# Optimization experiments

Hardware: AMD Instinct MI355X
Metric: run time of the kernel (lower is better)

Reference implementation:

```python
import jax, jax.numpy as jnp
import numpy as np

B, N, M, D = 8, 512, 64, 128
H = 64  # mlp_hidden_dim


def setup_inputs() -> dict:
    key = jax.random.key(0)
    ks = jax.random.split(key, 10)
    op_emb = jax.random.normal(ks[0], (B, N, D), dtype=jnp.float32)
    machine_emb = jax.random.normal(ks[1], (B, M, D), dtype=jnp.float32)
    edge_emb = jax.random.normal(ks[2], (B, N, M, D), dtype=jnp.float32)
    action_mask = jax.random.randint(ks[3], (B, N, M), 0, 2) > 0
    s1 = 1.0 / np.sqrt(3 * D)
    s2 = 1.0 / np.sqrt(H)
    W1 = jax.random.uniform(ks[4], (3 * D, H), jnp.float32, -s1, s1)
    b1 = jax.random.uniform(ks[5], (H,), jnp.float32, -s1, s1)
    W2 = jax.random.uniform(ks[6], (H, H), jnp.float32, -s2, s2)
    b2 = jax.random.uniform(ks[7], (H,), jnp.float32, -s2, s2)
    W3 = jax.random.uniform(ks[8], (H, 1), jnp.float32, -s2, s2)
    b3 = jax.random.uniform(ks[9], (1,), jnp.float32, -s2, s2)
    return {"op_emb": op_emb, "machine_emb": machine_emb, "edge_emb": edge_emb,
            "action_mask": action_mask,
            "W1": W1, "b1": b1, "W2": W2, "b2": b2, "W3": W3, "b3": b3}


def reference(op_emb, machine_emb, edge_emb, action_mask, W1, b1, W2, b2, W3, b3):
    # Split first linear over the three concat chunks to avoid materializing
    # the (B,N,M,3D) concat tensor (same math as cat -> Linear).
    Wo, Wm, We = W1[:D], W1[D:2 * D], W1[2 * D:]
    h = (jnp.einsum('bnd,dh->bnh', op_emb, Wo)[:, :, None, :]
         + jnp.einsum('bmd,dh->bmh', machine_emb, Wm)[:, None, :, :]
         + jnp.einsum('bnmd,dh->bnmh', edge_emb, We) + b1)  # (B,N,M,H)
    h = jax.nn.relu(h)
    h = jax.nn.relu(h @ W2 + b2)
    scores = (h @ W3 + b3)[..., 0]  # (B,N,M)
    scores = jnp.where(action_mask, scores, -jnp.inf)
    return jax.nn.log_softmax(scores.reshape(B, N * M), axis=-1)
```

## Files before the change

kernel.cpp:

```cpp
#include <hip/hip_runtime.h>
#include <math.h>

#define Bb 8
#define Nn 512
#define Mm 64
#define Dd 128
#define Hh 64
#define Gg 8
#define NEG_BIG (-1.0e30f)

typedef __bf16 bf16x8 __attribute__((ext_vector_type(8)));
typedef float  f32x4  __attribute__((ext_vector_type(4)));

#define WS_WEB   0u
#define WS_W2B   16384u
#define WS_CWSF  24576u
#define WS_AOP   155648u
#define WS_SCORE 1204224u
#define WS_PART  2252800u

#define GLOAD_LDS(gp, lp) __builtin_amdgcn_global_load_lds( \
    (const __attribute__((address_space(1))) void*)(gp),    \
    (__attribute__((address_space(3))) void*)(lp), 16, 0, 0)

__global__ __launch_bounds__(256) void prep_kernel(
    const float* __restrict__ W1, const float* __restrict__ W2,
    const float* __restrict__ op_emb, const float* __restrict__ machine_emb,
    const float* __restrict__ b1, char* __restrict__ ws)
{
    if (blockIdx.x < 48) {
        __bf16* WeB = (__bf16*)(ws + WS_WEB);
        __bf16* W2B = (__bf16*)(ws + WS_W2B);
        int idx = blockIdx.x * 256 + threadIdx.x;
        if (idx < 8192) {
            int fid = idx >> 9, rem = idx & 511;
            int lane = rem >> 3, j = rem & 7;
            int t = fid >> 2, ks = fid & 3;
            int q = lane >> 4, ln = lane & 15;
            int d = ks * 32 + q * 8 + j;
            int h = t * 16 + ln;
            WeB[idx] = (__bf16)W1[(size_t)(2 * Dd + d) * Hh + h];
        } else {
            int i2 = idx - 8192;
            int fid = i2 >> 9, rem = i2 & 511;
            int lane = rem >> 3, j = rem & 7;
            int t = fid >> 1, ks = fid & 1;
            int q = lane >> 4, ln = lane & 15;
            int k = ks * 32 + q * 8 + j;
            int h = t * 16 + ln;
            W2B[i2] = (__bf16)W2[(size_t)k * Hh + h];
        }
        return;
    }
    float* CwsF = (float*)(ws + WS_CWSF);
    float* Aop  = (float*)(ws + WS_AOP);
    const int bid = (blockIdx.x - 48) * 4 + (threadIdx.x >> 6);
    const int h = threadIdx.x & 63;
    if (bid < Bb * Mm) {
        const float* mg = machine_emb + (size_t)bid * Dd;
        const float* Wm = W1 + (size_t)Dd * Hh;
        float acc = b1[h];
#pragma unroll 8
        for (int d = 0; d < Dd; ++d) acc = fmaf(mg[d], Wm[d * Hh + h], acc);
        int b = bid >> 6, m = bid & 63;
        int wq = m >> 4, q = (m >> 2) & 3, r = m & 3;
        int t = h >> 4, ln = h & 15;
        CwsF[((((b * 4 + wq) * 4 + t) * 64) + (q * 16 + ln)) * 4 + r] = acc;
    } else {
        const int bn = bid - Bb * Mm;
        const float* og = op_emb + (size_t)bn * Dd;
        float acc = 0.f;
#pragma unroll 8
        for (int d = 0; d < Dd; ++d) acc = fmaf(og[d], W1[d * Hh + h], acc);
        Aop[(size_t)bn * Hh + h] = acc;
    }
}

__global__ __launch_bounds__(256, 2) void main_kernel(
    const float* __restrict__ edge_emb, const int* __restrict__ mask,
    const float* __restrict__ b2, const float* __restrict__ W3,
    const float* __restrict__ b3, char* __restrict__ ws)
{
    __shared__ float  sEdge[4 * 2 * 2048];
    __shared__ float  sAop[Gg * Hh];
    __shared__ int    sMask[Gg * Mm];
    __shared__ __bf16 sH1[Mm * 72];
    __shared__ float  sRed[8];

    float* scores = (float*)(ws + WS_SCORE);
    float* part   = (float*)(ws + WS_PART);

    const int tid  = threadIdx.x;
    const int lane = tid & 63;
    const int w    = tid >> 6;
    const int q    = lane >> 4;
    const int ln   = lane & 15;
    const int bn0  = blockIdx.x * Gg;
    const int b    = bn0 >> 9;
    const int wu   = __builtin_amdgcn_readfirstlane(w);

    const float* ebase = edge_emb + ((size_t)bn0 * Mm + w * 16 + ln) * Dd + q * 8;

    {
        float* d0 = &sEdge[(wu * 2 + 0) * 2048];
        float* d1 = &sEdge[(wu * 2 + 1) * 2048];
#pragma unroll
        for (int s = 0; s < 8; ++s)
            GLOAD_LDS(ebase + (s >> 1) * 32 + (s & 1) * 4, d0 + s * 256);
#pragma unroll
        for (int s = 0; s < 8; ++s)
            GLOAD_LDS(ebase + 8192 + (s >> 1) * 32 + (s & 1) * 4, d1 + s * 256);
    }

    if (tid < 128) {
        ((f32x4*)sAop)[tid] = ((const f32x4*)(ws + WS_AOP))[(size_t)bn0 * 16 + tid];
        ((int4*)sMask)[tid] = ((const int4*)mask)[(size_t)bn0 * 16 + tid];
    }

    bf16x8 weF[16], w2F[8];
    f32x4  cv[4];
    {
        const bf16x8* WeB = (const bf16x8*)(ws + WS_WEB);
        const bf16x8* W2B = (const bf16x8*)(ws + WS_W2B);
#pragma unroll
        for (int f = 0; f < 16; ++f) weF[f] = WeB[f * 64 + lane];
#pragma unroll
        for (int f = 0; f < 8; ++f)  w2F[f] = W2B[f * 64 + lane];
        const f32x4* CwsF = (const f32x4*)(ws + WS_CWSF) + (size_t)b * 1024;
#pragma unroll
        for (int t = 0; t < 4; ++t)  cv[t] = CwsF[(w * 4 + t) * 64 + lane];
    }

    float b2v[4], w3v[4];
#pragma unroll
    for (int t = 0; t < 4; ++t) { b2v[t] = b2[t * 16 + ln]; w3v[t] = W3[t * 16 + ln]; }
    const float bias3 = b3[0];

    float m_loc = NEG_BIG, l_loc = 0.f;

    __syncthreads();

#pragma unroll
    for (int g = 0; g < Gg; ++g) {
        const int buf = g & 1;
        const float* ldsrd = &sEdge[(wu * 2 + buf) * 2048];

        if (g == Gg - 1) __builtin_amdgcn_s_waitcnt(0x0F70);
        else             __builtin_amdgcn_s_waitcnt(0x0F78);

        f32x4 lo[4], hi[4];
#pragma unroll
        for (int ks = 0; ks < 4; ++ks) {
            lo[ks] = *(const f32x4*)&ldsrd[(ks * 2 + 0) * 256 + lane * 4];
            hi[ks] = *(const f32x4*)&ldsrd[(ks * 2 + 1) * 256 + lane * 4];
        }
        bf16x8 af[4];
#pragma unroll
        for (int ks = 0; ks < 4; ++ks) {
            bf16x8 a;
            a[0] = (__bf16)lo[ks][0]; a[1] = (__bf16)lo[ks][1];
            a[2] = (__bf16)lo[ks][2]; a[3] = (__bf16)lo[ks][3];
            a[4] = (__bf16)hi[ks][0]; a[5] = (__bf16)hi[ks][1];
            a[6] = (__bf16)hi[ks][2]; a[7] = (__bf16)hi[ks][3];
            af[ks] = a;
        }

        if (g + 2 < Gg) {
            float* dst = &sEdge[(wu * 2 + buf) * 2048];
            const float* src = ebase + (size_t)(g + 2) * 8192;
#pragma unroll
            for (int s = 0; s < 8; ++s)
                GLOAD_LDS(src + (s >> 1) * 32 + (s & 1) * 4, dst + s * 256);
        }

        f32x4 acc[4];
#pragma unroll
        for (int t = 0; t < 4; ++t) {
            float av = sAop[g * Hh + t * 16 + ln];
            acc[t][0] = cv[t][0] + av; acc[t][1] = cv[t][1] + av;
            acc[t][2] = cv[t][2] + av; acc[t][3] = cv[t][3] + av;
        }

#pragma unroll
        for (int t = 0; t < 4; ++t)
#pragma unroll
            for (int ks = 0; ks < 4; ++ks)
                acc[t] = __builtin_amdgcn_mfma_f32_16x16x32_bf16(af[ks], weF[t * 4 + ks], acc[t], 0, 0, 0);

#pragma unroll
        for (int t = 0; t < 4; ++t)
#pragma unroll
            for (int r = 0; r < 4; ++r)
                sH1[(w * 16 + q * 4 + r) * 72 + t * 16 + ln] =
                    (__bf16)fmaxf(acc[t][r], 0.f);

        bf16x8 a2[2];
#pragma unroll
        for (int ks = 0; ks < 2; ++ks)
            a2[ks] = *(const bf16x8*)&sH1[(w * 16 + ln) * 72 + ks * 32 + q * 8];
        f32x4 c2[4];
#pragma unroll
        for (int t = 0; t < 4; ++t) c2[t] = (f32x4){0.f, 0.f, 0.f, 0.f};
#pragma unroll
        for (int t = 0; t < 4; ++t)
#pragma unroll
            for (int ks = 0; ks < 2; ++ks)
                c2[t] = __builtin_amdgcn_mfma_f32_16x16x32_bf16(a2[ks], w2F[t * 2 + ks], c2[t], 0, 0, 0);

        float p[4] = {0.f, 0.f, 0.f, 0.f};
#pragma unroll
        for (int t = 0; t < 4; ++t)
#pragma unroll
            for (int r = 0; r < 4; ++r)
                p[r] += fmaxf(c2[t][r] + b2v[t], 0.f) * w3v[t];
#pragma unroll
        for (int r = 0; r < 4; ++r) {
            p[r] += __shfl_xor(p[r], 1, 64);
            p[r] += __shfl_xor(p[r], 2, 64);
            p[r] += __shfl_xor(p[r], 4, 64);
            p[r] += __shfl_xor(p[r], 8, 64);
        }
        const int m0 = w * 16 + q * 4;
        const int* mrow = &sMask[g * Mm + m0];
        float vv[4];
#pragma unroll
        for (int r = 0; r < 4; ++r) {
            float v = p[r] + bias3;
            vv[r] = mrow[r] ? v : NEG_BIG;
            if (mrow[r]) {
                float mn = fmaxf(m_loc, v);
                l_loc = l_loc * expf(m_loc - mn) + expf(v - mn);
                m_loc = mn;
            }
        }
        if (ln == 0) {
            float4 o; o.x = vv[0]; o.y = vv[1]; o.z = vv[2]; o.w = vv[3];
            *(float4*)&scores[(size_t)(bn0 + g) * Mm + m0] = o;
        }
    }

#pragma unroll
    for (int off = 16; off <= 32; off <<= 1) {
        float mo = __shfl_xor(m_loc, off, 64);
        float lo2 = __shfl_xor(l_loc, off, 64);
        float mn = fmaxf(m_loc, mo);
        l_loc = l_loc * expf(m_loc - mn) + lo2 * expf(mo - mn);
        m_loc = mn;
    }
    if (lane == 0) { sRed[w * 2] = m_loc; sRed[w * 2 + 1] = l_loc; }
    __syncthreads();
    if (tid == 0) {
        float gm = sRed[0], gl = sRed[1];
#pragma unroll
        for (int k = 1; k < 4; ++k) {
            float mo = sRed[k * 2], lo2 = sRed[k * 2 + 1];
            float mn = fmaxf(gm, mo);
            gl = gl * expf(gm - mn) + lo2 * expf(mo - mn);
            gm = mn;
        }
        float2 o; o.x = gm; o.y = gl;
        *(float2*)&part[blockIdx.x * 2] = o;
    }
}

__global__ __launch_bounds__(256) void lsm_apply_kernel(
    const char* __restrict__ ws, float* __restrict__ out)
{
    const float4* s4 = (const float4*)(ws + WS_SCORE);
    const float* part = (const float*)(ws + WS_PART);
    __shared__ float sCC;
    const int tid = threadIdx.x;
    const int b = blockIdx.x >> 5;
    if (tid < 64) {
        float2 p = *(const float2*)&part[(b * 64 + tid) * 2];
        float gm = p.x;
#pragma unroll
        for (int off = 1; off < 64; off <<= 1) gm = fmaxf(gm, __shfl_xor(gm, off, 64));
        float l = p.y * expf(p.x - gm);
#pragma unroll
        for (int off = 1; off < 64; off <<= 1) l += __shfl_xor(l, off, 64);
        if (tid == 0) sCC = gm + logf(l);
    }
    __syncthreads();
    const float c = sCC;
    const int i = blockIdx.x * 256 + tid;
    float4 v = s4[i];
    v.x -= c; v.y -= c; v.z -= c; v.w -= c;
    ((float4*)out)[i] = v;
}

extern "C" void kernel_launch(void* const* d_in, const int* in_sizes, int n_in,
                              void* d_out, int out_size, void* d_ws, size_t ws_size,
                              hipStream_t stream)
{
    const float* op_emb      = (const float*)d_in[0];
    const float* machine_emb = (const float*)d_in[1];
    const float* edge_emb    = (const float*)d_in[2];
    const int*   mask        = (const int*)  d_in[3];
    const float* W1 = (const float*)d_in[4];
    const float* b1 = (const float*)d_in[5];
    const float* W2 = (const float*)d_in[6];
    const float* b2 = (const float*)d_in[7];
    const float* W3 = (const float*)d_in[8];
    const float* b3 = (const float*)d_in[9];
    char* ws = (char*)d_ws;

    prep_kernel<<<48 + 1152, 256, 0, stream>>>(W1, W2, op_emb, machine_emb, b1, ws);
    main_kernel<<<(Bb * Nn) / Gg, 256, 0, stream>>>(edge_emb, mask, b2, W3, b3, ws);
    lsm_apply_kernel<<<256, 256, 0, stream>>>(ws, (float*)d_out);
}
```

Baseline: 227.2 us.

## Process one op row per block with direct register loads instead of LDS pipeline

The main kernel now launches one block per (b,n) row instead of batching eight rows per block. The double-buffered global-to-LDS prefetch pipeline is replaced by direct float4 loads into registers. The aim is more blocks and higher occupancy, since LDS use drops sharply, letting the hardware hide latency. The trade-off is that each block reloads all weight fragments for a single row, which adds redundant weight traffic and launch overhead. The log-softmax combine kernel is changed to reduce the now 512 partials per batch across a full block.

```diff
diff --git a/kernel.cpp b/kernel.cpp
--- a/kernel.cpp
+++ b/kernel.cpp
@@ -6,7 +6,6 @@
 #define Mm 64
 #define Dd 128
 #define Hh 64
-#define Gg 8
 #define NEG_BIG (-1.0e30f)
 
 typedef __bf16 bf16x8 __attribute__((ext_vector_type(8)));
@@ -18,10 +17,6 @@
 #define WS_AOP   155648u
 #define WS_SCORE 1204224u
 #define WS_PART  2252800u
-
-#define GLOAD_LDS(gp, lp) __builtin_amdgcn_global_load_lds( \
-    (const __attribute__((address_space(1))) void*)(gp),    \
-    (__attribute__((address_space(3))) void*)(lp), 16, 0, 0)
 
 __global__ __launch_bounds__(256) void prep_kernel(
     const float* __restrict__ W1, const float* __restrict__ W2,
@@ -81,9 +76,6 @@
     const float* __restrict__ b2, const float* __restrict__ W3,
     const float* __restrict__ b3, char* __restrict__ ws)
 {
-    __shared__ float  sEdge[4 * 2 * 2048];
-    __shared__ float  sAop[Gg * Hh];
-    __shared__ int    sMask[Gg * Mm];
     __shared__ __bf16 sH1[Mm * 72];
     __shared__ float  sRed[8];
 
@@ -95,30 +87,17 @@
     const int w    = tid >> 6;
     const int q    = lane >> 4;
     const int ln   = lane & 15;
-    const int bn0  = blockIdx.x * Gg;
-    const int b    = bn0 >> 9;
-    const int wu   = __builtin_amdgcn_readfirstlane(w);
-
-    const float* ebase = edge_emb + ((size_t)bn0 * Mm + w * 16 + ln) * Dd + q * 8;
-
-    {
-        float* d0 = &sEdge[(wu * 2 + 0) * 2048];
-        float* d1 = &sEdge[(wu * 2 + 1) * 2048];
-#pragma unroll
-        for (int s = 0; s < 8; ++s)
-            GLOAD_LDS(ebase + (s >> 1) * 32 + (s & 1) * 4, d0 + s * 256);
-#pragma unroll
-        for (int s = 0; s < 8; ++s)
-            GLOAD_LDS(ebase + 8192 + (s >> 1) * 32 + (s & 1) * 4, d1 + s * 256);
-    }
-
-    if (tid < 128) {
-        ((f32x4*)sAop)[tid] = ((const f32x4*)(ws + WS_AOP))[(size_t)bn0 * 16 + tid];
-        ((int4*)sMask)[tid] = ((const int4*)mask)[(size_t)bn0 * 16 + tid];
-    }
-
+    const int bn   = blockIdx.x;
+    const int b    = bn >> 9;
+
+    const float* Eg = edge_emb + (size_t)bn * (Mm * Dd) + (w * 16 + ln) * Dd + q * 8;
+    float4 raw[8];
+#pragma unroll
+    for (int ks = 0; ks < 4; ++ks) {
+        raw[2 * ks]     = *(const float4*)&Eg[ks * 32];
+        raw[2 * ks + 1] = *(const float4*)&Eg[ks * 32 + 4];
+    }
     bf16x8 weF[16], w2F[8];
-    f32x4  cv[4];
     {
         const bf16x8* WeB = (const bf16x8*)(ws + WS_WEB);
         const bf16x8* W2B = (const bf16x8*)(ws + WS_W2B);
@@ -126,108 +105,87 @@
         for (int f = 0; f < 16; ++f) weF[f] = WeB[f * 64 + lane];
 #pragma unroll
         for (int f = 0; f < 8; ++f)  w2F[f] = W2B[f * 64 + lane];
+    }
+    f32x4 cv[4];
+    {
         const f32x4* CwsF = (const f32x4*)(ws + WS_CWSF) + (size_t)b * 1024;
 #pragma unroll
-        for (int t = 0; t < 4; ++t)  cv[t] = CwsF[(w * 4 + t) * 64 + lane];
-    }
-
+        for (int t = 0; t < 4; ++t) cv[t] = CwsF[(w * 4 + t) * 64 + lane];
+    }
+    const float* Aop = (const float*)(ws + WS_AOP) + (size_t)bn * Hh;
+    float aopv[4];
+#pragma unroll
+    for (int t = 0; t < 4; ++t) aopv[t] = Aop[t * 16 + ln];
+    const int4 mk = *(const int4*)&mask[(size_t)bn * Mm + w * 16 + q * 4];
     float b2v[4], w3v[4];
 #pragma unroll
     for (int t = 0; t < 4; ++t) { b2v[t] = b2[t * 16 + ln]; w3v[t] = W3[t * 16 + ln]; }
     const float bias3 = b3[0];
 
+    bf16x8 af[4];
+#pragma unroll
+    for (int ks = 0; ks < 4; ++ks) {
+        float4 lo = raw[2 * ks], hi = raw[2 * ks + 1];
+        bf16x8 a;
+        a[0] = (__bf16)lo.x; a[1] = (__bf16)lo.y; a[2] = (__bf16)lo.z; a[3] = (__bf16)lo.w;
+        a[4] = (__bf16)hi.x; a[5] = (__bf16)hi.y; a[6] = (__bf16)hi.z; a[7] = (__bf16)hi.w;
+        af[ks] = a;
+    }
+
+    f32x4 acc[4];
+#pragma unroll
+    for (int t = 0; t < 4; ++t) {
+        acc[t][0] = cv[t][0] + aopv[t]; acc[t][1] = cv[t][1] + aopv[t];
+        acc[t][2] = cv[t][2] + aopv[t]; acc[t][3] = cv[t][3] + aopv[t];
+    }
+#pragma unroll
+    for (int t = 0; t < 4; ++t)
+#pragma unroll
+        for (int ks = 0; ks < 4; ++ks)
+            acc[t] = __builtin_amdgcn_mfma_f32_16x16x32_bf16(af[ks], weF[t * 4 + ks], acc[t], 0, 0, 0);
+
+#pragma unroll
+    for (int t = 0; t < 4; ++t)
+#pragma unroll
+        for (int r = 0; r < 4; ++r)
+            sH1[(w * 16 + q * 4 + r) * 72 + t * 16 + ln] = (__bf16)fmaxf(acc[t][r], 0.f);
+
+    bf16x8 a2[2];
+#pragma unroll
+    for (int ks = 0; ks < 2; ++ks)
+        a2[ks] = *(const bf16x8*)&sH1[(w * 16 + ln) * 72 + ks * 32 + q * 8];
+    f32x4 c2[4];
+#pragma unroll
+    for (int t = 0; t < 4; ++t) c2[t] = (f32x4){0.f, 0.f, 0.f, 0.f};
+#pragma unroll
+    for (int t = 0; t < 4; ++t)
+#pragma unroll
+        for (int ks = 0; ks < 2; ++ks)
+            c2[t] = __builtin_amdgcn_mfma_f32_16x16x32_bf16(a2[ks], w2F[t * 2 + ks], c2[t], 0, 0, 0);
+
+    float p[4] = {0.f, 0.f, 0.f, 0.f};
+#pragma unroll
+    for (int t = 0; t < 4; ++t)
+#pragma unroll
+        for (int r = 0; r < 4; ++r)
+            p[r] += fmaxf(c2[t][r] + b2v[t], 0.f) * w3v[t];
+#pragma unroll
+    for (int r = 0; r < 4; ++r) {
+        p[r] += __shfl_xor(p[r], 1, 64);
+        p[r] += __shfl_xor(p[r], 2, 64);
+        p[r] += __shfl_xor(p[r], 4, 64);
+        p[r] += __shfl_xor(p[r], 8, 64);
+    }
     float m_loc = NEG_BIG, l_loc = 0.f;
-
-    __syncthreads();
-
-#pragma unroll
-    for (int g = 0; g < Gg; ++g) {
-        const int buf = g & 1;
-        const float* ldsrd = &sEdge[(wu * 2 + buf) * 2048];
-
-        if (g == Gg - 1) __builtin_amdgcn_s_waitcnt(0x0F70);
-        else             __builtin_amdgcn_s_waitcnt(0x0F78);
-
-        f32x4 lo[4], hi[4];
-#pragma unroll
-        for (int ks = 0; ks < 4; ++ks) {
-            lo[ks] = *(const f32x4*)&ldsrd[(ks * 2 + 0) * 256 + lane * 4];
-            hi[ks] = *(const f32x4*)&ldsrd[(ks * 2 + 1) * 256 + lane * 4];
-        }
-        bf16x8 af[4];
-#pragma unroll
-        for (int ks = 0; ks < 4; ++ks) {
-            bf16x8 a;
-            a[0] = (__bf16)lo[ks][0]; a[1] = (__bf16)lo[ks][1];
-            a[2] = (__bf16)lo[ks][2]; a[3] = (__bf16)lo[ks][3];
-            a[4] = (__bf16)hi[ks][0]; a[5] = (__bf16)hi[ks][1];
-            a[6] = (__bf16)hi[ks][2]; a[7] = (__bf16)hi[ks][3];
-            af[ks] = a;
-        }
-
-        if (g + 2 < Gg) {
-            float* dst = &sEdge[(wu * 2 + buf) * 2048];
-            const float* src = ebase + (size_t)(g + 2) * 8192;
-#pragma unroll
-            for (int s = 0; s < 8; ++s)
-                GLOAD_LDS(src + (s >> 1) * 32 + (s & 1) * 4, dst + s * 256);
-        }
-
-        f32x4 acc[4];
-#pragma unroll
-        for (int t = 0; t < 4; ++t) {
-            float av = sAop[g * Hh + t * 16 + ln];
-            acc[t][0] = cv[t][0] + av; acc[t][1] = cv[t][1] + av;
-            acc[t][2] = cv[t][2] + av; acc[t][3] = cv[t][3] + av;
-        }
-
-#pragma unroll
-        for (int t = 0; t < 4; ++t)
-#pragma unroll
-            for (int ks = 0; ks < 4; ++ks)
-                acc[t] = __builtin_amdgcn_mfma_f32_16x16x32_bf16(af[ks], weF[t * 4 + ks], acc[t], 0, 0, 0);
-
-#pragma unroll
-        for (int t = 0; t < 4; ++t)
-#pragma unroll
-            for (int r = 0; r < 4; ++r)
-                sH1[(w * 16 + q * 4 + r) * 72 + t * 16 + ln] =
-                    (__bf16)fmaxf(acc[t][r], 0.f);
-
-        bf16x8 a2[2];
-#pragma unroll
-        for (int ks = 0; ks < 2; ++ks)
-            a2[ks] = *(const bf16x8*)&sH1[(w * 16 + ln) * 72 + ks * 32 + q * 8];
-        f32x4 c2[4];
-#pragma unroll
-        for (int t = 0; t < 4; ++t) c2[t] = (f32x4){0.f, 0.f, 0.f, 0.f};
-#pragma unroll
-        for (int t = 0; t < 4; ++t)
-#pragma unroll
-            for (int ks = 0; ks < 2; ++ks)
-                c2[t] = __builtin_amdgcn_mfma_f32_16x16x32_bf16(a2[ks], w2F[t * 2 + ks], c2[t], 0, 0, 0);
-
-        float p[4] = {0.f, 0.f, 0.f, 0.f};
-#pragma unroll
-        for (int t = 0; t < 4; ++t)
-#pragma unroll
-            for (int r = 0; r < 4; ++r)
-                p[r] += fmaxf(c2[t][r] + b2v[t], 0.f) * w3v[t];
-#pragma unroll
-        for (int r = 0; r < 4; ++r) {
-            p[r] += __shfl_xor(p[r], 1, 64);
-            p[r] += __shfl_xor(p[r], 2, 64);
-            p[r] += __shfl_xor(p[r], 4, 64);
-            p[r] += __shfl_xor(p[r], 8, 64);
-        }
-        const int m0 = w * 16 + q * 4;
-        const int* mrow = &sMask[g * Mm + m0];
+    const int m0 = w * 16 + q * 4;
+    {
+        const int mkv[4] = {mk.x, mk.y, mk.z, mk.w};
         float vv[4];
 #pragma unroll
         for (int r = 0; r < 4; ++r) {
             float v = p[r] + bias3;
-            vv[r] = mrow[r] ? v : NEG_BIG;
-            if (mrow[r]) {
+            vv[r] = mkv[r] ? v : NEG_BIG;
+            if (mkv[r]) {
                 float mn = fmaxf(m_loc, v);
                 l_loc = l_loc * expf(m_loc - mn) + expf(v - mn);
                 m_loc = mn;
@@ -235,10 +193,9 @@
         }
         if (ln == 0) {
             float4 o; o.x = vv[0]; o.y = vv[1]; o.z = vv[2]; o.w = vv[3];
-            *(float4*)&scores[(size_t)(bn0 + g) * Mm + m0] = o;
-        }
-    }
-
+            *(float4*)&scores[(size_t)bn * Mm + m0] = o;
+        }
+    }
 #pragma unroll
     for (int off = 16; off <= 32; off <<= 1) {
         float mo = __shfl_xor(m_loc, off, 64);
@@ -259,7 +216,7 @@
             gm = mn;
         }
         float2 o; o.x = gm; o.y = gl;
-        *(float2*)&part[blockIdx.x * 2] = o;
+        *(float2*)&part[bn * 2] = o;
     }
 }
 
@@ -268,18 +225,36 @@
 {
     const float4* s4 = (const float4*)(ws + WS_SCORE);
     const float* part = (const float*)(ws + WS_PART);
+    __shared__ float sComb[8];
     __shared__ float sCC;
     const int tid = threadIdx.x;
     const int b = blockIdx.x >> 5;
-    if (tid < 64) {
-        float2 p = *(const float2*)&part[(b * 64 + tid) * 2];
-        float gm = p.x;
-#pragma unroll
-        for (int off = 1; off < 64; off <<= 1) gm = fmaxf(gm, __shfl_xor(gm, off, 64));
-        float l = p.y * expf(p.x - gm);
-#pragma unroll
-        for (int off = 1; off < 64; off <<= 1) l += __shfl_xor(l, off, 64);
-        if (tid == 0) sCC = gm + logf(l);
+    {
+        float4 v = *(const float4*)&part[(size_t)b * 1024 + tid * 4];
+        float mn = fmaxf(v.x, v.z);
+        float m_loc = mn;
+        float l_loc = v.y * expf(v.x - mn) + v.w * expf(v.z - mn);
+#pragma unroll
+        for (int off = 1; off < 64; off <<= 1) {
+            float mo = __shfl_xor(m_loc, off, 64);
+            float lo2 = __shfl_xor(l_loc, off, 64);
+            float nm = fmaxf(m_loc, mo);
+            l_loc = l_loc * expf(m_loc - nm) + lo2 * expf(mo - nm);
+            m_loc = nm;
+        }
+        if ((tid & 63) == 0) { sComb[(tid >> 6) * 2] = m_loc; sComb[(tid >> 6) * 2 + 1] = l_loc; }
+    }
+    __syncthreads();
+    if (tid == 0) {
+        float gm = sComb[0], gl = sComb[1];
+#pragma unroll
+        for (int k = 1; k < 4; ++k) {
+            float mo = sComb[k * 2], lo2 = sComb[k * 2 + 1];
+            float mn = fmaxf(gm, mo);
+            gl = gl * expf(gm - mn) + lo2 * expf(mo - mn);
+            gm = mn;
+        }
+        sCC = gm + logf(gl);
     }
     __syncthreads();
     const float c = sCC;
@@ -306,6 +281,6 @@
     char* ws = (char*)d_ws;
 
     prep_kernel<<<48 + 1152, 256, 0, stream>>>(W1, W2, op_emb, machine_emb, b1, ws);
-    main_kernel<<<(Bb * Nn) / Gg, 256, 0, stream>>>(edge_emb, mask, b2, W3, b3, ws);
+    main_kernel<<<Bb * Nn, 256, 0, stream>>>(edge_emb, mask, b2, W3, b3, ws);
     lsm_apply_kernel<<<256, 256, 0, stream>>>(ws, (float*)d_out);
 }
```

Measured after the change: 237.2 us. +4.4%, slower.
